# Kernel optimization log

Measured on AMD Instinct MI355X. Metric: run time of the kernel, lower is better.

The kernel has to match this reference:

```python
import jax, jax.numpy as jnp
import numpy as np

B, S, D = 4, 1024, 2048
NH, NKV, HD = 16, 8, 128
N_EXP, TOP_K, RANK, ALPHA = 4, 2, 16, 32
LORA_SCALE = ALPHA / RANK
EPS = 1e-6
NEG_INF = -1e9


def setup_inputs() -> dict:
    key = jax.random.key(0)
    ks = jax.random.split(key, 12)
    inv_freq = 1.0 / (10000.0 ** (jnp.arange(0, HD, 2, dtype=jnp.float32) / HD))
    pos = jnp.arange(S, dtype=jnp.float32)
    freqs = pos[:, None] * inv_freq[None, :]            # [S, HD/2]
    emb = jnp.concatenate([freqs, freqs], axis=-1)      # [S, HD]
    cos = jnp.broadcast_to(jnp.cos(emb)[None], (B, S, HD))
    sin = jnp.broadcast_to(jnp.sin(emb)[None], (B, S, HD))
    s = 0.02
    return {
        "hidden_states": jax.random.normal(ks[0], (B, S, D), jnp.float32),
        "cos": cos,
        "sin": sin,
        "Wq": jax.random.normal(ks[1], (NH * HD, D), jnp.float32) * s,
        "Wk": jax.random.normal(ks[2], (NKV * HD, D), jnp.float32) * s,
        "Wv": jax.random.normal(ks[3], (NKV * HD, D), jnp.float32) * s,
        "Wo": jax.random.normal(ks[4], (D, NH * HD), jnp.float32) * s,
        "q_norm_w": jnp.ones((HD,), jnp.float32),
        "k_norm_w": jnp.ones((HD,), jnp.float32),
        "gate_w": jax.random.normal(ks[5], (N_EXP, D), jnp.float32) * s,
        "loraA": jax.random.normal(ks[6], (N_EXP, RANK, NH * HD), jnp.float32) * s,
        "loraB": jax.random.normal(ks[7], (N_EXP, D, RANK), jnp.float32) * s,
    }


def _rms_norm(x, w):
    # per-head-dim RMSNorm (Qwen3 style), computed in fp32
    var = jnp.mean(jnp.square(x.astype(jnp.float32)), axis=-1, keepdims=True)
    return (x.astype(jnp.float32) * jax.lax.rsqrt(var + EPS)).astype(x.dtype) * w


def _rotate_half(x):
    x1, x2 = jnp.split(x, 2, axis=-1)
    return jnp.concatenate([-x2, x1], axis=-1)


def reference(hidden_states, cos, sin, Wq, Wk, Wv, Wo, q_norm_w, k_norm_w, gate_w, loraA, loraB):
    b, s, d = hidden_states.shape
    scaling = HD ** -0.5

    # ---- router (top-k of softmax over 4 experts) ----
    flat = hidden_states.reshape(-1, d)                       # [T, D]
    router_logits = flat @ gate_w.T                           # [T, E]
    probs = jax.nn.softmax(router_logits.astype(jnp.float32), axis=-1)
    top_w, top_idx = jax.lax.top_k(probs, TOP_K)              # [T, K]
    top_w = top_w.astype(hidden_states.dtype)
    # dense per-expert weight: [T, E]
    expert_w = jnp.sum(jax.nn.one_hot(top_idx, N_EXP, dtype=top_w.dtype) * top_w[..., None], axis=1)

    # ---- QKV projections + per-head RMSNorm ----
    q = (hidden_states @ Wq.T).reshape(b, s, NH, HD)
    k = (hidden_states @ Wk.T).reshape(b, s, NKV, HD)
    v = (hidden_states @ Wv.T).reshape(b, s, NKV, HD)
    q = _rms_norm(q, q_norm_w).transpose(0, 2, 1, 3)          # [B, NH, S, HD]
    k = _rms_norm(k, k_norm_w).transpose(0, 2, 1, 3)          # [B, NKV, S, HD]
    v = v.transpose(0, 2, 1, 3)

    # ---- RoPE ----
    c, sn = cos[:, None], sin[:, None]                        # [B, 1, S, HD]
    q = q * c + _rotate_half(q) * sn
    k = k * c + _rotate_half(k) * sn

    # ---- GQA repeat + eager attention ----
    n_rep = NH // NKV
    k = jnp.repeat(k, n_rep, axis=1)
    v = jnp.repeat(v, n_rep, axis=1)
    attn = jnp.einsum('bhqd,bhkd->bhqk', q, k) * scaling
    causal = jnp.tril(jnp.ones((s, s), bool))
    attn = jnp.where(causal[None, None], attn, NEG_INF)
    attn_w = jax.nn.softmax(attn.astype(jnp.float32), axis=-1).astype(q.dtype)
    attn_out = jnp.einsum('bhqk,bhkd->bqhd', attn_w, v).reshape(b, s, NH * HD)

    # ---- base output projection + LoRA expert mixture ----
    base = attn_out @ Wo.T                                    # [B, S, D]
    x = attn_out.reshape(-1, NH * HD)                         # [T, NH*HD]
    h = jnp.einsum('td,erd->ter', x, loraA)                   # [T, E, R]
    delta = jnp.einsum('ter,edr->ted', h, loraB) * LORA_SCALE # [T, E, D]
    expert_out = jnp.einsum('te,ted->td', expert_w, delta).reshape(b, s, d)

    return base + expert_out
```

## Files before the change

### kernel.cpp

```cpp
#include <hip/hip_runtime.h>
#include <hip/hip_bf16.h>

#define S_LEN   1024
#define BATCH   4
#define DMODEL  2048
#define NHEADS  16
#define NKVH    8
#define HEADD   128
#define NTOK    4096
#define QKV_CH  4096

typedef __bf16 bf16x8 __attribute__((ext_vector_type(8)));
typedef float  f32x4  __attribute__((ext_vector_type(4)));

__device__ __forceinline__ float bf2f(unsigned short u) {
    return __uint_as_float(((unsigned)u) << 16);
}
__device__ __forceinline__ ushort f2bu(float f) {
    union { __hip_bfloat16 h; ushort u; } c;
    c.h = __float2bfloat16(f);
    return c.u;
}
__device__ __forceinline__ void gl_lds16(const ushort* g, ushort* l) {
    __builtin_amdgcn_global_load_lds(
        (const __attribute__((address_space(1))) void*)g,
        (__attribute__((address_space(3))) void*)l,
        16, 0, 0);
}

__global__ __launch_bounds__(256) void wcast_kernel(const float* __restrict__ Wq,
                                                    const float* __restrict__ Wk,
                                                    const float* __restrict__ Wv,
                                                    const float* __restrict__ Wo,
                                                    const float* __restrict__ lA,
                                                    __hip_bfloat16* __restrict__ wqkv,
                                                    __hip_bfloat16* __restrict__ wo,
                                                    __hip_bfloat16* __restrict__ acat) {
    int i = blockIdx.x * 256 + threadIdx.x;
    const float* src; __hip_bfloat16* dst; int off;
    if (i < 1048576)      { src = Wq; dst = wqkv;           off = i; }
    else if (i < 1572864) { src = Wk; dst = wqkv + 4194304; off = i - 1048576; }
    else if (i < 2097152) { src = Wv; dst = wqkv + 6291456; off = i - 1572864; }
    else if (i < 3145728) { src = Wo; dst = wo;             off = i - 2097152; }
    else if (i < 3178496) { src = lA; dst = acat;           off = i - 3145728; }
    else return;
    float4 v = ((const float4*)src)[off];
    union { ushort4 u; __hip_bfloat16 h[4]; } r;
    r.h[0] = __float2bfloat16(v.x);
    r.h[1] = __float2bfloat16(v.y);
    r.h[2] = __float2bfloat16(v.z);
    r.h[3] = __float2bfloat16(v.w);
    ((ushort4*)dst)[off] = r.u;
}

__global__ __launch_bounds__(256) void btrans_kernel(const float* __restrict__ lB,
                                                     const float* __restrict__ cosb,
                                                     const float* __restrict__ sinb,
                                                     ushort* __restrict__ Bt,
                                                     float4* __restrict__ cs4) {
    if (blockIdx.x < 512) {
        int idx = blockIdx.x * 256 + threadIdx.x;
        int d = idx >> 6, er = idx & 63;
        int e = er >> 4, r = er & 15;
        Bt[idx] = f2bu(lB[((size_t)e * DMODEL + d) * 16 + r]);
    } else {
        int idx = (blockIdx.x - 512) * 256 + threadIdx.x;
        int s = idx >> 6, d0 = idx & 63;
        const float* cp = cosb + (size_t)s * HEADD;
        const float* sp = sinb + (size_t)s * HEADD;
        cs4[idx] = make_float4(cp[d0], cp[d0 + 64], sp[d0], sp[d0 + 64]);
    }
}

__global__ __launch_bounds__(256) void gatecast_kernel(const float* __restrict__ X,
                                                       const float* __restrict__ GW,
                                                       __hip_bfloat16* __restrict__ Xb,
                                                       float* __restrict__ EW) {
    __shared__ float red[4][257];
    const int t = blockIdx.x, tid = threadIdx.x;
    const float* x = X + (size_t)t * DMODEL;
    __hip_bfloat16* xb = Xb + (size_t)t * DMODEL;
    float p0 = 0.f, p1 = 0.f, p2 = 0.f, p3 = 0.f;
#pragma unroll
    for (int c = 0; c < 2; c++) {
        int i4 = tid + c * 256;
        float4 v = ((const float4*)x)[i4];
        union { ushort4 u; __hip_bfloat16 h[4]; } r;
        r.h[0] = __float2bfloat16(v.x);
        r.h[1] = __float2bfloat16(v.y);
        r.h[2] = __float2bfloat16(v.z);
        r.h[3] = __float2bfloat16(v.w);
        ((ushort4*)xb)[i4] = r.u;
        int d = i4 * 4;
        const float* g0 = GW + d;
        p0 += v.x * g0[0] + v.y * g0[1] + v.z * g0[2] + v.w * g0[3];
        const float* g1 = GW + DMODEL + d;
        p1 += v.x * g1[0] + v.y * g1[1] + v.z * g1[2] + v.w * g1[3];
        const float* g2 = GW + 2 * DMODEL + d;
        p2 += v.x * g2[0] + v.y * g2[1] + v.z * g2[2] + v.w * g2[3];
        const float* g3 = GW + 3 * DMODEL + d;
        p3 += v.x * g3[0] + v.y * g3[1] + v.z * g3[2] + v.w * g3[3];
    }
    red[0][tid] = p0; red[1][tid] = p1; red[2][tid] = p2; red[3][tid] = p3;
    __syncthreads();
    for (int s = 128; s > 0; s >>= 1) {
        if (tid < s) {
            red[0][tid] += red[0][tid + s];
            red[1][tid] += red[1][tid + s];
            red[2][tid] += red[2][tid + s];
            red[3][tid] += red[3][tid + s];
        }
        __syncthreads();
    }
    if (tid == 0) {
        float l[4] = { red[0][0], red[1][0], red[2][0], red[3][0] };
        float mx = fmaxf(fmaxf(l[0], l[1]), fmaxf(l[2], l[3]));
        float pe[4], sum = 0.f;
        for (int e = 0; e < 4; e++) { pe[e] = __expf(l[e] - mx); sum += pe[e]; }
        float inv = 1.0f / sum;
        for (int e = 0; e < 4; e++) pe[e] *= inv;
        int i1 = 0;
        for (int e = 1; e < 4; e++) if (pe[e] > pe[i1]) i1 = e;
        int i2 = -1;
        for (int e = 0; e < 4; e++) if (e != i1 && (i2 < 0 || pe[e] > pe[i2])) i2 = e;
        float o[4] = {0.f, 0.f, 0.f, 0.f};
        o[i1] = pe[i1]; o[i2] = pe[i2];
        float* ew = EW + (size_t)t * 4;
        ew[0] = o[0]; ew[1] = o[1]; ew[2] = o[2]; ew[3] = o[3];
    }
}

#define LDSA0 0
#define LDSB0 16384
#define LDSA1 32768
#define LDSB1 49152

#define FENCE_BAR() do { asm volatile("" ::: "memory"); __builtin_amdgcn_s_barrier(); } while (0)

__device__ __forceinline__ void stage_half(const ushort* src, ushort* dst, int ld) {
    gl_lds16(src, dst);
    gl_lds16(src + (size_t)64 * ld, dst + 4096);
}

#define PHASE_MFMA_PRE()  do { \
    asm volatile("" ::: "memory"); \
    __builtin_amdgcn_s_barrier(); \
    asm volatile("s_waitcnt lgkmcnt(0)" ::: "memory"); \
    __builtin_amdgcn_sched_barrier(0); \
    __builtin_amdgcn_s_setprio(1); } while (0)

#define PHASE_MFMA_POST() do { \
    __builtin_amdgcn_s_setprio(0); } while (0)

__device__ __forceinline__ void ktile(const ushort* As, const ushort* Bs,
                                      f32x4 (&acc)[8][4],
                                      int aBase, int bBase, int cs0, int cs1,
                                      const ushort* s1s, ushort* s1d, bool s12en,
                                      const ushort* s2s, ushort* s2d,
                                      const ushort* s3s, ushort* s3d, bool s34en,
                                      const ushort* s4s, ushort* s4d,
                                      int K, bool lastVm)
{
    bf16x8 a0[4][2], a1[4][2], b0[2][2], b1[2][2];

#pragma unroll
    for (int ii = 0; ii < 4; ii++) {
        a0[ii][0] = *(const bf16x8*)(As + aBase + ii * 2048 + cs0);
        a0[ii][1] = *(const bf16x8*)(As + aBase + ii * 2048 + cs1);
    }
#pragma unroll
    for (int jj = 0; jj < 2; jj++) {
        b0[jj][0] = *(const bf16x8*)(Bs + bBase + jj * 4096 + cs0);
        b0[jj][1] = *(const bf16x8*)(Bs + bBase + jj * 4096 + cs1);
    }
    if (s12en) stage_half(s1s, s1d, K);
    asm volatile("s_waitcnt lgkmcnt(8)" ::: "memory");
    PHASE_MFMA_PRE();
#pragma unroll
    for (int k = 0; k < 2; k++)
#pragma unroll
        for (int ii = 0; ii < 4; ii++)
#pragma unroll
            for (int jj = 0; jj < 2; jj++)
                acc[ii][2 * jj] = __builtin_amdgcn_mfma_f32_16x16x32_bf16(
                    a0[ii][k], b0[jj][k], acc[ii][2 * jj], 0, 0, 0);
    PHASE_MFMA_POST();
    FENCE_BAR();

#pragma unroll
    for (int jj = 0; jj < 2; jj++) {
        b1[jj][0] = *(const bf16x8*)(Bs + bBase + 8192 + jj * 4096 + cs0);
        b1[jj][1] = *(const bf16x8*)(Bs + bBase + 8192 + jj * 4096 + cs1);
    }
    if (s12en) stage_half(s2s, s2d, K);
    PHASE_MFMA_PRE();
#pragma unroll
    for (int k = 0; k < 2; k++)
#pragma unroll
        for (int ii = 0; ii < 4; ii++)
#pragma unroll
            for (int jj = 0; jj < 2; jj++)
                acc[ii][1 + 2 * jj] = __builtin_amdgcn_mfma_f32_16x16x32_bf16(
                    a0[ii][k], b1[jj][k], acc[ii][1 + 2 * jj], 0, 0, 0);
    PHASE_MFMA_POST();
    FENCE_BAR();

#pragma unroll
    for (int ii = 0; ii < 4; ii++) {
        a1[ii][0] = *(const bf16x8*)(As + aBase + 8192 + ii * 2048 + cs0);
        a1[ii][1] = *(const bf16x8*)(As + aBase + 8192 + ii * 2048 + cs1);
    }
    if (s34en) stage_half(s3s, s3d, K);
    PHASE_MFMA_PRE();
#pragma unroll
    for (int k = 0; k < 2; k++)
#pragma unroll
        for (int ii = 0; ii < 4; ii++)
#pragma unroll
            for (int jj = 0; jj < 2; jj++)
                acc[4 + ii][2 * jj] = __builtin_amdgcn_mfma_f32_16x16x32_bf16(
                    a1[ii][k], b0[jj][k], acc[4 + ii][2 * jj], 0, 0, 0);
    PHASE_MFMA_POST();
    FENCE_BAR();

    if (s34en) stage_half(s4s, s4d, K);
    asm volatile("" ::: "memory");
    __builtin_amdgcn_s_barrier();
    __builtin_amdgcn_sched_barrier(0);
    __builtin_amdgcn_s_setprio(1);
#pragma unroll
    for (int k = 0; k < 2; k++)
#pragma unroll
        for (int ii = 0; ii < 4; ii++)
#pragma unroll
            for (int jj = 0; jj < 2; jj++)
                acc[4 + ii][1 + 2 * jj] = __builtin_amdgcn_mfma_f32_16x16x32_bf16(
                    a1[ii][k], b1[jj][k], acc[4 + ii][1 + 2 * jj], 0, 0, 0);
    __builtin_amdgcn_s_setprio(0);
    if (lastVm) { asm volatile("s_waitcnt vmcnt(0)" ::: "memory"); }
    else        { asm volatile("s_waitcnt vmcnt(4)" ::: "memory"); }
    __builtin_amdgcn_s_barrier();
}

__global__ __launch_bounds__(512, 2) void gemm256(const ushort* __restrict__ A,
                                                  const ushort* __restrict__ B,
                                                  const float4* __restrict__ cs4,
                                                  const float* __restrict__ qnw,
                                                  const float* __restrict__ knw,
                                                  ushort* __restrict__ Qb,
                                                  ushort* __restrict__ Kb,
                                                  ushort* __restrict__ Vt,
                                                  int K) {
    __shared__ __align__(16) ushort lds[65536];
    const int tid  = threadIdx.x;
    const int wave = tid >> 6, lane = tid & 63;
    const int l16  = lane & 15, quad = lane >> 4;
    const int wm = wave >> 2, wn = wave & 3;

    const int wg0 = blockIdx.x;
    const int swz = (wg0 & 7) * 32 + (wg0 >> 3);
    const int m0 = (swz >> 4) * 256, n0 = (swz & 15) * 256;

    const int srow = tid >> 3;
    const int scol = ((tid & 7) * 8) ^ ((srow & 7) << 3);
    const ushort* aSrc = A + (size_t)(m0 + srow) * K + scol;
    const ushort* bSrc = B + (size_t)(n0 + srow) * K + scol;

    const int aBase = (wm * 16 + l16) * 64;
    const int bBase = (wn * 16 + l16) * 64;
    const int cs0 = ((0 + quad) ^ (l16 & 7)) * 8;
    const int cs1 = ((4 + quad) ^ (l16 & 7)) * 8;

    f32x4 acc[8][4];
#pragma unroll
    for (int i = 0; i < 8; i++)
#pragma unroll
        for (int j = 0; j < 4; j++) acc[i][j] = (f32x4){0.f, 0.f, 0.f, 0.f};

    const int NT = K >> 6;

    const ushort* A0s = lds + LDSA0;
    const ushort* B0s = lds + LDSB0;
    const ushort* A1s = lds + LDSA1;
    const ushort* B1s = lds + LDSB1;

    stage_half(aSrc,                     lds + LDSA0 + tid * 8, K);
    stage_half(aSrc + (size_t)128 * K,   lds + LDSA0 + 8192 + tid * 8, K);
    stage_half(bSrc,                     lds + LDSB0 + tid * 8, K);
    stage_half(bSrc + (size_t)128 * K,   lds + LDSB0 + 8192 + tid * 8, K);
    stage_half(aSrc + 64,                lds + LDSA1 + tid * 8, K);
    stage_half(bSrc + 64,                lds + LDSB1 + tid * 8, K);
    asm volatile("s_waitcnt vmcnt(4)" ::: "memory");
    __builtin_amdgcn_s_barrier();

    for (int t = 0; t + 1 < NT; t += 2) {
        const bool s34 = (t + 2) < NT, s78 = (t + 3) < NT;
        const int k1 = (t + 1) * 64, k2 = (t + 2) * 64, k3 = (t + 3) * 64;

        ktile(A0s, B0s, acc, aBase, bBase, cs0, cs1,
              aSrc + (size_t)128 * K + k1, lds + LDSA1 + 8192 + tid * 8, true,
              bSrc + (size_t)128 * K + k1, lds + LDSB1 + 8192 + tid * 8,
              aSrc + k2,                   lds + LDSA0 + tid * 8, s34,
              bSrc + k2,                   lds + LDSB0 + tid * 8,
              K, !s34);

        ktile(A1s, B1s, acc, aBase, bBase, cs0, cs1,
              aSrc + (size_t)128 * K + k2, lds + LDSA0 + 8192 + tid * 8, s34,
              bSrc + (size_t)128 * K + k2, lds + LDSB0 + 8192 + tid * 8,
              aSrc + k3,                   lds + LDSA1 + tid * 8, s78,
              bSrc + k3,                   lds + LDSB1 + tid * 8,
              K, !s78);
    }

    const int nb = n0 >> 8;
    if (nb < 12) {
        const bool isQ = (nb < 8);
        const float scale = isQ ? 0.08838834764831845f : 1.0f;
        const float* nw = isQ ? qnw : knw;
        const int d0 = wn * 16 + l16;
        const float w0 = nw[d0] * scale, w1 = nw[d0 + 64] * scale;
        const int h0 = isQ ? (n0 >> 7) : ((n0 - 2048) >> 7);
        const int nh = isQ ? 16 : 8;
        ushort* gbase = isQ ? Qb : Kb;
        float* fsq = (float*)(lds + 32768);
        const float4* cvrow = cs4 + ((m0 & 1023) * 64 + d0);

#pragma unroll
        for (int half = 0; half < 2; half++) {
#pragma unroll
            for (int i2 = 0; i2 < 4; i2++)
#pragma unroll
                for (int r = 0; r < 4; r++) {
                    const int i = half * 4 + i2;
                    const int r128 = i2 * 32 + wm * 16 + quad * 4 + r;
#pragma unroll
                    for (int h = 0; h < 2; h++) {
                        float x1 = acc[i][h][r], x2 = acc[i][h + 2][r];
                        float p = x1 * x1 + x2 * x2;
                        p += __shfl_xor(p, 1);
                        p += __shfl_xor(p, 2);
                        p += __shfl_xor(p, 4);
                        p += __shfl_xor(p, 8);
                        if (l16 == 0) fsq[(r128 * 2 + h) * 4 + wn] = p;
                    }
                }
            __syncthreads();

#pragma unroll
            for (int i2 = 0; i2 < 4; i2++)
#pragma unroll
                for (int r = 0; r < 4; r++) {
                    const int i = half * 4 + i2;
                    const int r128 = i2 * 32 + wm * 16 + quad * 4 + r;
                    const float4 cv = cvrow[(size_t)(half * 128 + r128) * 64];
                    const int sw = ((r128 >> 2) & 3) << 4;
                    ushort* lrow = lds + r128 * 256;
#pragma unroll
                    for (int h = 0; h < 2; h++) {
                        const float* q4 = fsq + (r128 * 2 + h) * 4;
                        float ssq = q4[0] + q4[1] + q4[2] + q4[3];
                        float rstd = rsqrtf(ssq * (1.0f / 128.0f) + 1e-6f);
                        float n1 = acc[i][h][r] * rstd * w0;
                        float n2 = acc[i][h + 2][r] * rstd * w1;
                        lrow[(h * 128 + d0) ^ sw]      = f2bu(n1 * cv.x - n2 * cv.z);
                        lrow[(h * 128 + d0 + 64) ^ sw] = f2bu(n2 * cv.y + n1 * cv.w);
                    }
                }
            __syncthreads();

#pragma unroll
            for (int g = 0; g < 8; g++) {
                int gg = tid + g * 512;
                int row = gg >> 5, colg = gg & 31;
                int col8 = colg * 8;
                int sw = ((row >> 2) & 3) << 4;
                uint4 v = *(const uint4*)(lds + row * 256 + (col8 ^ sw));
                int head = col8 >> 7, d = col8 & 127;
                int tok = m0 + half * 128 + row;
                int b = tok >> 10, s = tok & 1023;
                *(uint4*)(gbase + ((size_t)((b * nh + h0 + head) * 1024 + s)) * HEADD + d) = v;
            }
            __syncthreads();
        }
    } else {
#pragma unroll
        for (int i = 0; i < 8; i++)
#pragma unroll
            for (int j = 0; j < 4; j++) {
                int coll = (j & 1) * 128 + (j >> 1) * 64 + wn * 16 + l16;
                int xr = (coll & 7) << 3;
#pragma unroll
                for (int r = 0; r < 4; r++) {
                    int rowl = (i & 3) * 32 + (i >> 2) * 128 + wm * 16 + quad * 4 + r;
                    lds[coll * 256 + (rowl ^ xr)] = f2bu(acc[i][j][r]);
                }
            }
        __syncthreads();
        const int b = m0 >> 10, s0 = m0 & 1023;
        const int kv0 = (n0 - 3072) >> 7;
#pragma unroll
        for (int g = 0; g < 16; g++) {
            int gg = tid + g * 512;
            int d = gg >> 5, sg = gg & 31;
            uint4 v = *(const uint4*)(lds + d * 256 + ((sg * 8) ^ ((d & 7) << 3)));
            int kv = kv0 + (d >> 7), dh = d & 127;
            *(uint4*)(Vt + ((size_t)((b * 8 + kv) * 128 + dh)) * 1024 + s0 + sg * 8) = v;
        }
    }
}

__global__ __launch_bounds__(256) void gemm_bt_lora(const ushort* __restrict__ A,
                                                    const ushort* __restrict__ B,
                                                    const ushort* __restrict__ A2,
                                                    const ushort* __restrict__ B2,
                                                    float* __restrict__ C) {
    __shared__ ushort As[128 * 32];
    __shared__ ushort Bs[128 * 32];
    const int tid  = threadIdx.x;
    const int wave = tid >> 6, lane = tid & 63;
    const int l16  = lane & 15, quad = lane >> 4;
    const int m0 = blockIdx.y * 128, n0 = blockIdx.x * 128;
    const int wm = (wave >> 1) * 64, wn = (wave & 1) * 64;
    const int K = DMODEL, N = DMODEL;

    f32x4 acc[4][4];
#pragma unroll
    for (int i = 0; i < 4; i++)
#pragma unroll
        for (int j = 0; j < 4; j++) acc[i][j] = (f32x4){0.f, 0.f, 0.f, 0.f};

    const int r1 = tid >> 2, kg1 = ((tid & 3) * 8) ^ ((( tid >> 2) & 3) << 3);
    const int r2 = (tid + 256) >> 2, kg2 = (((tid + 256) & 3) * 8) ^ ((((tid + 256) >> 2) & 3) << 3);
    const int csr = (quad * 8) ^ ((l16 & 3) << 3);

    for (int k0 = 0; k0 < K; k0 += 32) {
        __syncthreads();
        gl_lds16(A + (size_t)(m0 + r1) * K + k0 + kg1, As + tid * 8);
        gl_lds16(B + (size_t)(n0 + r1) * K + k0 + kg1, Bs + tid * 8);
        gl_lds16(A + (size_t)(m0 + r2) * K + k0 + kg2, As + (tid + 256) * 8);
        gl_lds16(B + (size_t)(n0 + r2) * K + k0 + kg2, Bs + (tid + 256) * 8);
        __syncthreads();
        bf16x8 af[4], bfr[4];
#pragma unroll
        for (int i = 0; i < 4; i++) {
            af[i]  = *(const bf16x8*)(As + (wm + i * 16 + l16) * 32 + csr);
            bfr[i] = *(const bf16x8*)(Bs + (wn + i * 16 + l16) * 32 + csr);
        }
#pragma unroll
        for (int i = 0; i < 4; i++)
#pragma unroll
            for (int j = 0; j < 4; j++)
                acc[i][j] = __builtin_amdgcn_mfma_f32_16x16x32_bf16(af[i], bfr[j], acc[i][j], 0, 0, 0);
    }

#pragma unroll
    for (int k0 = 0; k0 < 64; k0 += 32) {
        __syncthreads();
        gl_lds16(A2 + (size_t)(m0 + r1) * 64 + k0 + kg1, As + tid * 8);
        gl_lds16(B2 + (size_t)(n0 + r1) * 64 + k0 + kg1, Bs + tid * 8);
        gl_lds16(A2 + (size_t)(m0 + r2) * 64 + k0 + kg2, As + (tid + 256) * 8);
        gl_lds16(B2 + (size_t)(n0 + r2) * 64 + k0 + kg2, Bs + (tid + 256) * 8);
        __syncthreads();
        bf16x8 af[4], bfr[4];
#pragma unroll
        for (int i = 0; i < 4; i++) {
            af[i]  = *(const bf16x8*)(As + (wm + i * 16 + l16) * 32 + csr);
            bfr[i] = *(const bf16x8*)(Bs + (wn + i * 16 + l16) * 32 + csr);
        }
#pragma unroll
        for (int i = 0; i < 4; i++)
#pragma unroll
            for (int j = 0; j < 4; j++)
                acc[i][j] = __builtin_amdgcn_mfma_f32_16x16x32_bf16(af[i], bfr[j], acc[i][j], 0, 0, 0);
    }

#pragma unroll
    for (int i = 0; i < 4; i++)
#pragma unroll
        for (int j = 0; j < 4; j++)
#pragma unroll
            for (int r = 0; r < 4; r++) {
                int m = m0 + wm + i * 16 + quad * 4 + r;
                int n = n0 + wn + j * 16 + l16;
                C[(size_t)m * N + n] = acc[i][j][r];
            }
}

__global__ __launch_bounds__(256) void lora_h_kernel(const ushort* __restrict__ X,
                                                     const ushort* __restrict__ Acat,
                                                     const float* __restrict__ EW,
                                                     ushort* __restrict__ G) {
    __shared__ ushort As[64 * 64];
    __shared__ ushort Bs[64 * 64];
    const int tid = threadIdx.x;
    const int wave = tid >> 6, lane = tid & 63;
    const int l16 = lane & 15, quad = lane >> 4;
    const int m0 = blockIdx.x * 64;

    f32x4 acc[4];
#pragma unroll
    for (int nt = 0; nt < 4; nt++) acc[nt] = (f32x4){0.f, 0.f, 0.f, 0.f};

    const int r1 = tid >> 3;
    const int scol = ((tid & 7) * 8) ^ ((r1 & 7) << 3);
    const int cs0 = ((0 + quad) ^ (l16 & 7)) * 8;
    const int cs1 = ((4 + quad) ^ (l16 & 7)) * 8;

    for (int k0 = 0; k0 < DMODEL; k0 += 64) {
        __syncthreads();
        gl_lds16(X + (size_t)(m0 + r1) * DMODEL + k0 + scol, As + tid * 8);
        gl_lds16(X + (size_t)(m0 + 32 + r1) * DMODEL + k0 + scol, As + 2048 + tid * 8);
        gl_lds16(Acat + (size_t)r1 * DMODEL + k0 + scol, Bs + tid * 8);
        gl_lds16(Acat + (size_t)(32 + r1) * DMODEL + k0 + scol, Bs + 2048 + tid * 8);
        __syncthreads();
        bf16x8 af0 = *(const bf16x8*)(As + (wave * 16 + l16) * 64 + cs0);
        bf16x8 af1 = *(const bf16x8*)(As + (wave * 16 + l16) * 64 + cs1);
#pragma unroll
        for (int nt = 0; nt < 4; nt++) {
            bf16x8 b0 = *(const bf16x8*)(Bs + (nt * 16 + l16) * 64 + cs0);
            acc[nt] = __builtin_amdgcn_mfma_f32_16x16x32_bf16(af0, b0, acc[nt], 0, 0, 0);
            bf16x8 b1 = *(const bf16x8*)(Bs + (nt * 16 + l16) * 64 + cs1);
            acc[nt] = __builtin_amdgcn_mfma_f32_16x16x32_bf16(af1, b1, acc[nt], 0, 0, 0);
        }
    }
#pragma unroll
    for (int nt = 0; nt < 4; nt++)
#pragma unroll
        for (int r = 0; r < 4; r++) {
            int m = m0 + wave * 16 + quad * 4 + r;
            float wsc = 2.0f * EW[(size_t)m * 4 + nt];
            G[(size_t)m * 64 + nt * 16 + l16] = f2bu(acc[nt][r] * wsc);
        }
}

#define KPITCH 136
#define VPITCH 72
__global__ __launch_bounds__(256) void fattn_kernel(const ushort* __restrict__ Qb,
                                                    const ushort* __restrict__ Kb,
                                                    const ushort* __restrict__ Vt,
                                                    __hip_bfloat16* __restrict__ O) {
    __shared__ __align__(16) ushort Ks[64 * KPITCH];
    __shared__ __align__(16) ushort Vs[128 * VPITCH];
    __shared__ __align__(16) ushort Ps[4 * 16 * VPITCH];
    const int tid = threadIdx.x;
    const int wq = tid >> 6, lane = tid & 63;
    const int l16 = lane & 15, quad = lane >> 4;
    const int qblk = 15 - (blockIdx.x >> 6);
    const int bh = blockIdx.x & 63;
    const int b = bh >> 4, h = bh & 15;
    const int kvb = b * 8 + (h >> 1);
    const int q0 = qblk * 64;
    const int qbase = q0 + wq * 16;

    bf16x8 qf[4];
    const ushort* qrow = Qb + ((size_t)bh * S_LEN + qbase + l16) * HEADD;
#pragma unroll
    for (int kt = 0; kt < 4; kt++)
        qf[kt] = *(const bf16x8*)(qrow + kt * 32 + quad * 8);

    f32x4 oacc[8];
#pragma unroll
    for (int dt = 0; dt < 8; dt++) oacc[dt] = (f32x4){0.f, 0.f, 0.f, 0.f};
    float l[4] = { 0.f, 0.f, 0.f, 0.f };

    const ushort* kbase = Kb + (size_t)kvb * S_LEN * HEADD;
    const ushort* vbase = Vt + (size_t)kvb * HEADD * S_LEN;
    const int ntiles = qblk + 1;

    for (int kb = 0; kb < ntiles; kb++) {
        const int k0 = kb * 64;
        __syncthreads();
        for (int c = tid; c < 1024; c += 256) {
            int row = c >> 4, col = (c & 15) * 8;
            *(uint4*)(Ks + row * KPITCH + col) =
                *(const uint4*)(kbase + (size_t)(k0 + row) * HEADD + col);
        }
        for (int c = tid; c < 1024; c += 256) {
            int row = c >> 3, col = (c & 7) * 8;
            *(uint4*)(Vs + row * VPITCH + col) =
                *(const uint4*)(vbase + (size_t)row * S_LEN + k0 + col);
        }
        __syncthreads();

        f32x4 sacc[4];
#pragma unroll
        for (int nt = 0; nt < 4; nt++) sacc[nt] = (f32x4){0.f, 0.f, 0.f, 0.f};
#pragma unroll
        for (int kt = 0; kt < 4; kt++) {
#pragma unroll
            for (int nt = 0; nt < 4; nt++) {
                bf16x8 kf = *(const bf16x8*)(Ks + (nt * 16 + l16) * KPITCH + kt * 32 + quad * 8);
                sacc[nt] = __builtin_amdgcn_mfma_f32_16x16x32_bf16(qf[kt], kf, sacc[nt], 0, 0, 0);
            }
        }

#pragma unroll
        for (int r = 0; r < 4; r++) {
            const int qg = qbase + quad * 4 + r;
#pragma unroll
            for (int nt = 0; nt < 4; nt++) {
                int kg = k0 + nt * 16 + l16;
                float p = (kg <= qg) ? __expf(sacc[nt][r]) : 0.f;
                l[r] += p;
                Ps[wq * 16 * VPITCH + (quad * 4 + r) * VPITCH + nt * 16 + l16] = f2bu(p);
            }
        }

#pragma unroll
        for (int kt2 = 0; kt2 < 2; kt2++) {
            bf16x8 pf = *(const bf16x8*)(Ps + wq * 16 * VPITCH + l16 * VPITCH + kt2 * 32 + quad * 8);
#pragma unroll
            for (int dt = 0; dt < 8; dt++) {
                bf16x8 vf = *(const bf16x8*)(Vs + (dt * 16 + l16) * VPITCH + kt2 * 32 + quad * 8);
                oacc[dt] = __builtin_amdgcn_mfma_f32_16x16x32_bf16(pf, vf, oacc[dt], 0, 0, 0);
            }
        }
    }

#pragma unroll
    for (int r = 0; r < 4; r++) {
        float lr = l[r];
        lr += __shfl_xor(lr, 1);
        lr += __shfl_xor(lr, 2);
        lr += __shfl_xor(lr, 4);
        lr += __shfl_xor(lr, 8);
        float inv = 1.0f / lr;
        size_t base = ((size_t)(b * S_LEN + qbase + quad * 4 + r)) * (NHEADS * HEADD) + h * HEADD;
#pragma unroll
        for (int dt = 0; dt < 8; dt++)
            O[base + dt * 16 + l16] = __float2bfloat16(oacc[dt][r] * inv);
    }
}

extern "C" void kernel_launch(void* const* d_in, const int* in_sizes, int n_in,
                              void* d_out, int out_size, void* d_ws, size_t ws_size,
                              hipStream_t stream) {
    const float* hidden = (const float*)d_in[0];
    const float* cosb   = (const float*)d_in[1];
    const float* sinb   = (const float*)d_in[2];
    const float* Wq     = (const float*)d_in[3];
    const float* Wk     = (const float*)d_in[4];
    const float* Wv     = (const float*)d_in[5];
    const float* Wo     = (const float*)d_in[6];
    const float* qnw    = (const float*)d_in[7];
    const float* knw    = (const float*)d_in[8];
    const float* gw     = (const float*)d_in[9];
    const float* lA     = (const float*)d_in[10];
    const float* lB     = (const float*)d_in[11];
    float* out = (float*)d_out;

    char* ws = (char*)d_ws;
    __hip_bfloat16* hid_bf  = (__hip_bfloat16*)ws;
    __hip_bfloat16* wqkv_bf = (__hip_bfloat16*)(ws + (16u << 20));
    __hip_bfloat16* wo_bf   = (__hip_bfloat16*)(ws + (32u << 20));
    ushort*         Qb      = (ushort*)(ws + (40u << 20));
    ushort*         Kb      = (ushort*)(ws + (56u << 20));
    ushort*         Vt      = (ushort*)(ws + (64u << 20));
    __hip_bfloat16* attn_bf = (__hip_bfloat16*)(ws + (72u << 20));
    ushort*         Acat    = (ushort*)(ws + (104u << 20));
    ushort*         Bt      = (ushort*)(ws + (104u << 20) + (256u << 10));
    ushort*         G       = (ushort*)(ws + (104u << 20) + (512u << 10));
    float*          ew      = (float*)(ws + (105u << 20));
    float4*         cs4     = (float4*)(ws + (106u << 20));

    wcast_kernel<<<12416, 256, 0, stream>>>(Wq, Wk, Wv, Wo, lA,
                                            wqkv_bf, wo_bf, (__hip_bfloat16*)Acat);
    gatecast_kernel<<<4096, 256, 0, stream>>>(hidden, gw, hid_bf, ew);
    btrans_kernel<<<768, 256, 0, stream>>>(lB, cosb, sinb, Bt, cs4);

    gemm256<<<256, 512, 0, stream>>>((const ushort*)hid_bf, (const ushort*)wqkv_bf,
                                     cs4, qnw, knw, Qb, Kb, Vt, DMODEL);

    fattn_kernel<<<1024, 256, 0, stream>>>(Qb, Kb, Vt, attn_bf);

    lora_h_kernel<<<64, 256, 0, stream>>>((const ushort*)attn_bf, Acat, ew, G);

    gemm_bt_lora<<<dim3(16, 32), 256, 0, stream>>>((const ushort*)attn_bf, (const ushort*)wo_bf,
                                                   G, Bt, out);
}
```

Before: 361.0 us.

## Rewrite Wo GEMM as double-buffered 256x128 pipeline; async swizzled LDS loads in attention

Replaces the simple single-buffered 128x128 output-projection GEMM with a 512-thread, 256x128-tile kernel. It double-buffers LDS with global_load_lds prefetch of the next k-slices during MFMA phases, uses XOR-swizzled layouts, raises MFMA priority and remaps workgroups for L2 locality, with the LoRA tail folded into the same pipeline. The attention kernel switches K/V staging from register round-trip copies with padded pitch to direct global-to-LDS loads with XOR swizzle, and adds setprio around its MFMA blocks. The hand-tuned waitcnt counts and barriers raise the risk of synchronization errors in exchange for overlapping memory and compute.

```diff
diff --git a/kernel.cpp b/kernel.cpp
--- a/kernel.cpp
+++ b/kernel.cpp
@@ -137,7 +137,7 @@
 
 #define FENCE_BAR() do { asm volatile("" ::: "memory"); __builtin_amdgcn_s_barrier(); } while (0)
 
-__device__ __forceinline__ void stage_half(const ushort* src, ushort* dst, int ld) {
+__device__ __forceinline__ void stage_half(const ushort* src, ushort* dst, size_t ld) {
     gl_lds16(src, dst);
     gl_lds16(src + (size_t)64 * ld, dst + 4096);
 }
@@ -409,81 +409,151 @@
     }
 }
 
-__global__ __launch_bounds__(256) void gemm_bt_lora(const ushort* __restrict__ A,
-                                                    const ushort* __restrict__ B,
-                                                    const ushort* __restrict__ A2,
-                                                    const ushort* __restrict__ B2,
-                                                    float* __restrict__ C) {
-    __shared__ ushort As[128 * 32];
-    __shared__ ushort Bs[128 * 32];
+#define WO_A0 0
+#define WO_A1 16384
+#define WO_B0 32768
+#define WO_B1 40960
+
+__device__ __forceinline__ void wo_tile(const ushort* As, const ushort* Bs,
+                                        f32x4 (&acc)[8][2],
+                                        int aBase, int bBase, int cs0, int cs1,
+                                        const ushort* s1s, ushort* s1d, size_t s1ld, bool s1en,
+                                        const ushort* s2as, ushort* s2ad,
+                                        const ushort* s2bs, ushort* s2bd, size_t s2ld, bool s2en,
+                                        bool lastVm)
+{
+    bf16x8 a0[4][2], a1[4][2], b[2][2];
+
+#pragma unroll
+    for (int ii = 0; ii < 4; ii++) {
+        a0[ii][0] = *(const bf16x8*)(As + aBase + ii * 2048 + cs0);
+        a0[ii][1] = *(const bf16x8*)(As + aBase + ii * 2048 + cs1);
+    }
+#pragma unroll
+    for (int jj = 0; jj < 2; jj++) {
+        b[jj][0] = *(const bf16x8*)(Bs + bBase + jj * 4096 + cs0);
+        b[jj][1] = *(const bf16x8*)(Bs + bBase + jj * 4096 + cs1);
+    }
+    if (s1en) stage_half(s1s, s1d, s1ld);
+    asm volatile("s_waitcnt lgkmcnt(8)" ::: "memory");
+    PHASE_MFMA_PRE();
+#pragma unroll
+    for (int k = 0; k < 2; k++)
+#pragma unroll
+        for (int ii = 0; ii < 4; ii++)
+#pragma unroll
+            for (int jj = 0; jj < 2; jj++)
+                acc[ii][jj] = __builtin_amdgcn_mfma_f32_16x16x32_bf16(
+                    a0[ii][k], b[jj][k], acc[ii][jj], 0, 0, 0);
+    PHASE_MFMA_POST();
+    FENCE_BAR();
+
+#pragma unroll
+    for (int ii = 0; ii < 4; ii++) {
+        a1[ii][0] = *(const bf16x8*)(As + aBase + 8192 + ii * 2048 + cs0);
+        a1[ii][1] = *(const bf16x8*)(As + aBase + 8192 + ii * 2048 + cs1);
+    }
+    if (s2en) { stage_half(s2as, s2ad, s2ld); stage_half(s2bs, s2bd, s2ld); }
+    PHASE_MFMA_PRE();
+#pragma unroll
+    for (int k = 0; k < 2; k++)
+#pragma unroll
+        for (int ii = 0; ii < 4; ii++)
+#pragma unroll
+            for (int jj = 0; jj < 2; jj++)
+                acc[4 + ii][jj] = __builtin_amdgcn_mfma_f32_16x16x32_bf16(
+                    a1[ii][k], b[jj][k], acc[4 + ii][jj], 0, 0, 0);
+    PHASE_MFMA_POST();
+    if (lastVm) { asm volatile("s_waitcnt vmcnt(0)" ::: "memory"); }
+    else        { asm volatile("s_waitcnt vmcnt(4)" ::: "memory"); }
+    __builtin_amdgcn_s_barrier();
+}
+
+__global__ __launch_bounds__(512, 2) void gemm_wo(const ushort* __restrict__ A,
+                                                  const ushort* __restrict__ B,
+                                                  const ushort* __restrict__ A2,
+                                                  const ushort* __restrict__ B2,
+                                                  float* __restrict__ C) {
+    __shared__ __align__(16) ushort lds[49152];
     const int tid  = threadIdx.x;
     const int wave = tid >> 6, lane = tid & 63;
     const int l16  = lane & 15, quad = lane >> 4;
-    const int m0 = blockIdx.y * 128, n0 = blockIdx.x * 128;
-    const int wm = (wave >> 1) * 64, wn = (wave & 1) * 64;
+    const int wm = wave >> 2, wn = wave & 3;
     const int K = DMODEL, N = DMODEL;
 
-    f32x4 acc[4][4];
-#pragma unroll
-    for (int i = 0; i < 4; i++)
-#pragma unroll
-        for (int j = 0; j < 4; j++) acc[i][j] = (f32x4){0.f, 0.f, 0.f, 0.f};
-
-    const int r1 = tid >> 2, kg1 = ((tid & 3) * 8) ^ ((( tid >> 2) & 3) << 3);
-    const int r2 = (tid + 256) >> 2, kg2 = (((tid + 256) & 3) * 8) ^ ((((tid + 256) >> 2) & 3) << 3);
-    const int csr = (quad * 8) ^ ((l16 & 3) << 3);
-
-    for (int k0 = 0; k0 < K; k0 += 32) {
-        __syncthreads();
-        gl_lds16(A + (size_t)(m0 + r1) * K + k0 + kg1, As + tid * 8);
-        gl_lds16(B + (size_t)(n0 + r1) * K + k0 + kg1, Bs + tid * 8);
-        gl_lds16(A + (size_t)(m0 + r2) * K + k0 + kg2, As + (tid + 256) * 8);
-        gl_lds16(B + (size_t)(n0 + r2) * K + k0 + kg2, Bs + (tid + 256) * 8);
-        __syncthreads();
-        bf16x8 af[4], bfr[4];
-#pragma unroll
-        for (int i = 0; i < 4; i++) {
-            af[i]  = *(const bf16x8*)(As + (wm + i * 16 + l16) * 32 + csr);
-            bfr[i] = *(const bf16x8*)(Bs + (wn + i * 16 + l16) * 32 + csr);
-        }
-#pragma unroll
-        for (int i = 0; i < 4; i++)
-#pragma unroll
-            for (int j = 0; j < 4; j++)
-                acc[i][j] = __builtin_amdgcn_mfma_f32_16x16x32_bf16(af[i], bfr[j], acc[i][j], 0, 0, 0);
-    }
-
-#pragma unroll
-    for (int k0 = 0; k0 < 64; k0 += 32) {
-        __syncthreads();
-        gl_lds16(A2 + (size_t)(m0 + r1) * 64 + k0 + kg1, As + tid * 8);
-        gl_lds16(B2 + (size_t)(n0 + r1) * 64 + k0 + kg1, Bs + tid * 8);
-        gl_lds16(A2 + (size_t)(m0 + r2) * 64 + k0 + kg2, As + (tid + 256) * 8);
-        gl_lds16(B2 + (size_t)(n0 + r2) * 64 + k0 + kg2, Bs + (tid + 256) * 8);
-        __syncthreads();
-        bf16x8 af[4], bfr[4];
-#pragma unroll
-        for (int i = 0; i < 4; i++) {
-            af[i]  = *(const bf16x8*)(As + (wm + i * 16 + l16) * 32 + csr);
-            bfr[i] = *(const bf16x8*)(Bs + (wn + i * 16 + l16) * 32 + csr);
-        }
-#pragma unroll
-        for (int i = 0; i < 4; i++)
-#pragma unroll
-            for (int j = 0; j < 4; j++)
-                acc[i][j] = __builtin_amdgcn_mfma_f32_16x16x32_bf16(af[i], bfr[j], acc[i][j], 0, 0, 0);
-    }
-
-#pragma unroll
-    for (int i = 0; i < 4; i++)
-#pragma unroll
-        for (int j = 0; j < 4; j++)
-#pragma unroll
-            for (int r = 0; r < 4; r++) {
-                int m = m0 + wm + i * 16 + quad * 4 + r;
-                int n = n0 + wn + j * 16 + l16;
-                C[(size_t)m * N + n] = acc[i][j][r];
-            }
+    const int wg0 = blockIdx.x;
+    const int swz = (wg0 & 7) * 32 + (wg0 >> 3);
+    const int m0 = (swz >> 4) * 256, n0 = (swz & 15) * 128;
+
+    const int srow = tid >> 3;
+    const int scol = ((tid & 7) * 8) ^ ((srow & 7) << 3);
+    const ushort* aSrc  = A  + (size_t)(m0 + srow) * K + scol;
+    const ushort* bSrc  = B  + (size_t)(n0 + srow) * K + scol;
+    const ushort* a2Src = A2 + (size_t)(m0 + srow) * 64 + scol;
+    const ushort* b2Src = B2 + (size_t)(n0 + srow) * 64 + scol;
+
+    const int aBase = (wm * 16 + l16) * 64;
+    const int bBase = (wn * 16 + l16) * 64;
+    const int cs0 = ((0 + quad) ^ (l16 & 7)) * 8;
+    const int cs1 = ((4 + quad) ^ (l16 & 7)) * 8;
+
+    f32x4 acc[8][2];
+#pragma unroll
+    for (int i = 0; i < 8; i++)
+#pragma unroll
+        for (int j = 0; j < 2; j++) acc[i][j] = (f32x4){0.f, 0.f, 0.f, 0.f};
+
+    const ushort* A0s = lds + WO_A0;
+    const ushort* B0s = lds + WO_B0;
+    const ushort* A1s = lds + WO_A1;
+    const ushort* B1s = lds + WO_B1;
+
+    stage_half(aSrc,                   lds + WO_A0 + tid * 8, K);
+    stage_half(aSrc + (size_t)128 * K, lds + WO_A0 + 8192 + tid * 8, K);
+    stage_half(bSrc,                   lds + WO_B0 + tid * 8, K);
+    stage_half(aSrc + 64,              lds + WO_A1 + tid * 8, K);
+    stage_half(bSrc + 64,              lds + WO_B1 + tid * 8, K);
+    asm volatile("s_waitcnt vmcnt(4)" ::: "memory");
+    __builtin_amdgcn_s_barrier();
+
+    for (int t = 0; t < 32; t += 2) {
+        const int u1 = t + 1, u2 = t + 2, u3 = t + 3;
+        const bool l2 = (u2 == 32);
+        const bool s3en = (u3 <= 32);
+
+        const ushort* s2as = l2 ? a2Src : (aSrc + (size_t)u2 * 64);
+        const ushort* s2bs = l2 ? b2Src : (bSrc + (size_t)u2 * 64);
+        const size_t  s2ld = l2 ? (size_t)64 : (size_t)K;
+        wo_tile(A0s, B0s, acc, aBase, bBase, cs0, cs1,
+                aSrc + (size_t)128 * K + (size_t)u1 * 64, lds + WO_A1 + 8192 + tid * 8, K, true,
+                s2as, lds + WO_A0 + tid * 8,
+                s2bs, lds + WO_B0 + tid * 8, s2ld, true,
+                false);
+
+        const ushort* s1s = l2 ? (a2Src + (size_t)128 * 64)
+                               : (aSrc + (size_t)128 * K + (size_t)u2 * 64);
+        const size_t  s1ld = l2 ? (size_t)64 : (size_t)K;
+        wo_tile(A1s, B1s, acc, aBase, bBase, cs0, cs1,
+                s1s, lds + WO_A0 + 8192 + tid * 8, s1ld, true,
+                aSrc + (size_t)u3 * 64, lds + WO_A1 + tid * 8,
+                bSrc + (size_t)u3 * 64, lds + WO_B1 + tid * 8, K, s3en,
+                !s3en);
+    }
+    wo_tile(A0s, B0s, acc, aBase, bBase, cs0, cs1,
+            nullptr, nullptr, K, false,
+            nullptr, nullptr, nullptr, nullptr, K, false,
+            true);
+
+    float* crow = C + (size_t)(m0 + wm * 16 + quad * 4) * N + n0 + wn * 16 + l16;
+#pragma unroll
+    for (int i = 0; i < 8; i++) {
+        float* cpi = crow + (size_t)((i & 3) * 32 + (i >> 2) * 128) * N;
+#pragma unroll
+        for (int r = 0; r < 4; r++)
+#pragma unroll
+            for (int jj = 0; jj < 2; jj++)
+                cpi[(size_t)r * N + jj * 64] = acc[i][jj][r];
+    }
 }
 
 __global__ __launch_bounds__(256) void lora_h_kernel(const ushort* __restrict__ X,
@@ -533,14 +603,13 @@
         }
 }
 
-#define KPITCH 136
 #define VPITCH 72
 __global__ __launch_bounds__(256) void fattn_kernel(const ushort* __restrict__ Qb,
                                                     const ushort* __restrict__ Kb,
                                                     const ushort* __restrict__ Vt,
                                                     __hip_bfloat16* __restrict__ O) {
-    __shared__ __align__(16) ushort Ks[64 * KPITCH];
-    __shared__ __align__(16) ushort Vs[128 * VPITCH];
+    __shared__ __align__(16) ushort Ks[64 * 128];
+    __shared__ __align__(16) ushort Vs[128 * 64];
     __shared__ __align__(16) ushort Ps[4 * 16 * VPITCH];
     const int tid = threadIdx.x;
     const int wq = tid >> 6, lane = tid & 63;
@@ -567,32 +636,34 @@
     const ushort* vbase = Vt + (size_t)kvb * HEADD * S_LEN;
     const int ntiles = qblk + 1;
 
+    const int kr = tid >> 4, kc = ((tid & 15) * 8) ^ ((( tid >> 4) & 7) << 3);
+    const int vr = tid >> 3, vc = ((tid & 7) * 8) ^ ((( tid >> 3) & 7) << 3);
+    const int xrK = (l16 & 7) << 3;
+
     for (int kb = 0; kb < ntiles; kb++) {
         const int k0 = kb * 64;
         __syncthreads();
-        for (int c = tid; c < 1024; c += 256) {
-            int row = c >> 4, col = (c & 15) * 8;
-            *(uint4*)(Ks + row * KPITCH + col) =
-                *(const uint4*)(kbase + (size_t)(k0 + row) * HEADD + col);
-        }
-        for (int c = tid; c < 1024; c += 256) {
-            int row = c >> 3, col = (c & 7) * 8;
-            *(uint4*)(Vs + row * VPITCH + col) =
-                *(const uint4*)(vbase + (size_t)row * S_LEN + k0 + col);
-        }
-        __syncthreads();
+#pragma unroll
+        for (int c = 0; c < 4; c++) {
+            gl_lds16(kbase + (size_t)(k0 + c * 16 + kr) * HEADD + kc, Ks + c * 2048 + tid * 8);
+            gl_lds16(vbase + (size_t)(c * 32 + vr) * S_LEN + k0 + vc, Vs + c * 2048 + tid * 8);
+        }
+        asm volatile("s_waitcnt vmcnt(0)" ::: "memory");
+        __builtin_amdgcn_s_barrier();
 
         f32x4 sacc[4];
 #pragma unroll
         for (int nt = 0; nt < 4; nt++) sacc[nt] = (f32x4){0.f, 0.f, 0.f, 0.f};
+        __builtin_amdgcn_s_setprio(1);
 #pragma unroll
         for (int kt = 0; kt < 4; kt++) {
 #pragma unroll
             for (int nt = 0; nt < 4; nt++) {
-                bf16x8 kf = *(const bf16x8*)(Ks + (nt * 16 + l16) * KPITCH + kt * 32 + quad * 8);
+                bf16x8 kf = *(const bf16x8*)(Ks + (nt * 16 + l16) * 128 + ((kt * 32 + quad * 8) ^ xrK));
                 sacc[nt] = __builtin_amdgcn_mfma_f32_16x16x32_bf16(qf[kt], kf, sacc[nt], 0, 0, 0);
             }
         }
+        __builtin_amdgcn_s_setprio(0);
 
 #pragma unroll
         for (int r = 0; r < 4; r++) {
@@ -606,15 +677,17 @@
             }
         }
 
+        __builtin_amdgcn_s_setprio(1);
 #pragma unroll
         for (int kt2 = 0; kt2 < 2; kt2++) {
             bf16x8 pf = *(const bf16x8*)(Ps + wq * 16 * VPITCH + l16 * VPITCH + kt2 * 32 + quad * 8);
 #pragma unroll
             for (int dt = 0; dt < 8; dt++) {
-                bf16x8 vf = *(const bf16x8*)(Vs + (dt * 16 + l16) * VPITCH + kt2 * 32 + quad * 8);
+                bf16x8 vf = *(const bf16x8*)(Vs + (dt * 16 + l16) * 64 + ((kt2 * 32 + quad * 8) ^ xrK));
                 oacc[dt] = __builtin_amdgcn_mfma_f32_16x16x32_bf16(pf, vf, oacc[dt], 0, 0, 0);
             }
         }
+        __builtin_amdgcn_s_setprio(0);
     }
 
 #pragma unroll
@@ -675,6 +748,6 @@
 
     lora_h_kernel<<<64, 256, 0, stream>>>((const ushort*)attn_bf, Acat, ew, G);
 
-    gemm_bt_lora<<<dim3(16, 32), 256, 0, stream>>>((const ushort*)attn_bf, (const ushort*)wo_bf,
-                                                   G, Bt, out);
-}
+    gemm_wo<<<256, 512, 0, stream>>>((const ushort*)attn_bf, (const ushort*)wo_bf,
+                                     G, Bt, out);
+}
```

New measurement: 316.0 us. -12.5%, faster.
